# Optimization experiments

Measured on AMD Instinct MI355X. Metric: run time of the kernel, lower is better.

## Reference

```python
import jax, jax.numpy as jnp
import numpy as np

H = 8          # num_heads
WIN = 256      # window_size (even); half-window = 128
NEG = -1e30    # stand-in for -inf that keeps softmax grad finite


def setup_inputs() -> dict:
    key = jax.random.key(0)
    ks = jax.random.split(key, 6)
    B, S, D, E = 2, 2048, 512, 512
    x = jax.random.normal(ks[0], (B, S, D), dtype=jnp.float32)
    padding_mask = jax.random.randint(ks[1], (B, S), 0, 2, dtype=jnp.int32)
    Wqkv = jax.random.normal(ks[2], (3 * E, D), dtype=jnp.float32) * 0.02
    bqkv = jnp.zeros((3 * E,), dtype=jnp.float32)
    Wo = jax.random.normal(ks[3], (E, E), dtype=jnp.float32) * 0.02
    bo = jnp.zeros((E,), dtype=jnp.float32)
    return {"x": x, "padding_mask": padding_mask, "Wqkv": Wqkv, "bqkv": bqkv,
            "Wo": Wo, "bo": bo}


def reference(x, padding_mask, Wqkv, bqkv, Wo, bo):
    B, S, _ = x.shape
    E = Wo.shape[0]
    Dh = E // H
    # qkv projection -> [B, H, S, 3*Dh]
    qkv = (x @ Wqkv.T + bqkv).reshape(B, S, H, 3 * Dh).transpose(0, 2, 1, 3)
    q, k, v = jnp.split(qkv, 3, axis=-1)
    # full S x S scores (original materializes [B,H,S,S]); scale by sqrt(head_dim)
    scores = jnp.einsum('bhsd,bhtd->bhst', q, k) / jnp.sqrt(jnp.float32(Dh))
    # sliding-window band: |i - j| <= window_size // 2
    i = jnp.arange(S)[:, None]
    j = jnp.arange(S)[None, :]
    band = jnp.abs(i - j) <= (WIN // 2)               # [S, S]
    # padding: entry valid only if both row and col tokens are non-pad
    pad = padding_mask.astype(bool)                    # [B, S]
    valid = band[None, None] & pad[:, None, None, :] & pad[:, None, :, None]
    scores = jnp.where(valid, scores, NEG)
    A = jax.nn.softmax(scores, axis=-1)
    # rows with no valid entry -> nan_to_num(., 0) in original -> zeros here
    row_valid = jnp.any(valid, axis=-1, keepdims=True)
    A = jnp.where(row_valid, A, 0.0)
    Y = jnp.einsum('bhst,bhtd->bhsd', A, v)            # [B,H,S,Dh]
    Y = Y.transpose(0, 2, 1, 3).reshape(B, S, E)
    return Y @ Wo.T + bo
```

## Files before the change

kernel.cpp:

```cpp
#include <hip/hip_runtime.h>

#define NH   8
#define SEQ  2048
#define DIM  512
#define EMB  512
#define DH   64
#define HALF 128
#define QT   16
#define KW   272
#define SCS  276

typedef __attribute__((ext_vector_type(8))) short short8;
typedef __attribute__((ext_vector_type(4))) float f32x4;

__device__ __forceinline__ unsigned short f2bf(float f) {
    unsigned int u = __float_as_uint(f);
    return (unsigned short)((u + 0x7fffu + ((u >> 16) & 1u)) >> 16);
}

__device__ __forceinline__ unsigned cvtpk(float lo, float hi) {
    unsigned r;
    asm("v_cvt_pk_bf16_f32 %0, %1, %2" : "=v"(r) : "v"(lo), "v"(hi));
    return r;
}

__device__ __forceinline__ void gload_lds16(const void* g, void* l) {
    __builtin_amdgcn_global_load_lds((__attribute__((address_space(1))) void*)g,
                                     (__attribute__((address_space(3))) void*)l,
                                     16, 0, 0);
}

__global__ __launch_bounds__(256)
void gemm_qkv(const float* __restrict__ A, const float* __restrict__ B,
              const float* __restrict__ bias, unsigned short* __restrict__ qkvh,
              unsigned short* __restrict__ vT) {
    constexpr int BM = 128, BN = 64, BK = 64;
    __shared__ unsigned short As[BM * BK];
    __shared__ unsigned short Bs[BN * BK];
    const int bid = blockIdx.x;
    const int wg = (bid & 7) * 96 + (bid >> 3);
    const int bm = (wg / 24) * BM, bn = (wg % 24) * BN;
    const int t = threadIdx.x, lane = t & 63, wid = t >> 6;
    const int wr = wid >> 1, wc = wid & 1;
    const int lr = lane & 15, lg = lane >> 4;

    f32x4 acc[4][2];
    #pragma unroll
    for (int m = 0; m < 4; ++m)
        #pragma unroll
        for (int n = 0; n < 2; ++n)
            acc[m][n] = (f32x4){0.f, 0.f, 0.f, 0.f};

    for (int kt = 0; kt < DIM; kt += BK) {
        #pragma unroll
        for (int i = 0; i < 4; ++i) {
            const int c = t + 256 * i, r = c >> 3, c8 = c & 7;
            const float4* src = (const float4*)(A + (size_t)(bm + r) * DIM + kt + c8 * 8);
            const float4 v0 = src[0], v1 = src[1];
            const uint4 pk = make_uint4(cvtpk(v0.x, v0.y), cvtpk(v0.z, v0.w),
                                        cvtpk(v1.x, v1.y), cvtpk(v1.z, v1.w));
            *(uint4*)&As[r * 64 + ((c8 ^ (r & 7)) << 3)] = pk;
        }
        #pragma unroll
        for (int i = 0; i < 2; ++i) {
            const int c = t + 256 * i, r = c >> 3, c8 = c & 7;
            const float4* src = (const float4*)(B + (size_t)(bn + r) * DIM + kt + c8 * 8);
            const float4 v0 = src[0], v1 = src[1];
            const uint4 pk = make_uint4(cvtpk(v0.x, v0.y), cvtpk(v0.z, v0.w),
                                        cvtpk(v1.x, v1.y), cvtpk(v1.z, v1.w));
            *(uint4*)&Bs[r * 64 + ((c8 ^ (r & 7)) << 3)] = pk;
        }
        __syncthreads();
        short8 af[2][4], bf[2][2];
        #pragma unroll
        for (int kk = 0; kk < 2; ++kk) {
            #pragma unroll
            for (int m = 0; m < 4; ++m) {
                const int row = wr * 64 + m * 16 + lr;
                af[kk][m] = *(const short8*)&As[row * 64 + (((kk * 4 + lg) ^ (row & 7)) << 3)];
            }
            #pragma unroll
            for (int n = 0; n < 2; ++n) {
                const int row = wc * 32 + n * 16 + lr;
                bf[kk][n] = *(const short8*)&Bs[row * 64 + (((kk * 4 + lg) ^ (row & 7)) << 3)];
            }
        }
        #pragma unroll
        for (int kk = 0; kk < 2; ++kk)
            #pragma unroll
            for (int m = 0; m < 4; ++m)
                #pragma unroll
                for (int n = 0; n < 2; ++n)
                    acc[m][n] = __builtin_amdgcn_mfma_f32_16x16x32_bf16(af[kk][m], bf[kk][n], acc[m][n], 0, 0, 0);
        __syncthreads();
    }

    unsigned short* Tr = As;
    #pragma unroll
    for (int n = 0; n < 2; ++n) {
        const int cl = wc * 32 + n * 16 + lr;
        const float bv = bias[bn + cl];
        #pragma unroll
        for (int m = 0; m < 4; ++m)
            #pragma unroll
            for (int r = 0; r < 4; ++r)
                Tr[(wr * 64 + m * 16 + lg * 4 + r) * 72 + cl] = f2bf(acc[m][n][r] + bv);
    }
    __syncthreads();

    const int h = bn / 192, ty = (bn >> 6) % 3;
    const int bb = bm >> 11, s0 = bm & 2047;
    if (ty < 2) {
        unsigned short* plane = qkvh + (((size_t)(bb * NH + h) * 3 + ty) * SEQ) * DH;
        const int s = t >> 1, hf = (t & 1) * 32;
        unsigned short* dst = plane + (size_t)(s0 + s) * DH + hf;
        #pragma unroll
        for (int k8 = 0; k8 < 4; ++k8)
            *(short8*)&dst[k8 * 8] = *(const short8*)&Tr[s * 72 + hf + k8 * 8];
    } else {
        const int d = t >> 2, pp = t & 3;
        unsigned short* vrow = vT + ((size_t)(bb * NH + h) * DH + d) * SEQ + s0 + pp * 32;
        #pragma unroll
        for (int k8 = 0; k8 < 4; ++k8) {
            alignas(16) unsigned short tmp[8];
            #pragma unroll
            for (int k = 0; k < 8; ++k) tmp[k] = Tr[(pp * 32 + k8 * 8 + k) * 72 + d];
            *(short8*)&vrow[k8 * 8] = *(short8*)tmp;
        }
    }
}

__global__ __launch_bounds__(256)
void attn_mfma(const unsigned short* __restrict__ qkvh,
               const unsigned short* __restrict__ vT,
               const int* __restrict__ pad,
               unsigned short* __restrict__ Yb) {
    const int bid = blockIdx.x;
    const int wg = (bid & 7) * 256 + (bid >> 3);
    const int bh = wg >> 7, qt = wg & 127;
    const int b = bh >> 3, h = bh & 7;
    const int i0 = qt * QT, kb = i0 - HALF;
    const int t = threadIdx.x, lane = t & 63, w = t >> 6;
    const int lr = lane & 15, lg = lane >> 4;

    __shared__ float Sc[QT * SCS];

    const unsigned short* Qg = qkvh + ((size_t)bh * 3 + 0) * SEQ * DH;
    const unsigned short* Kg = qkvh + ((size_t)bh * 3 + 1) * SEQ * DH;
    const unsigned short* vTg = vT + (size_t)bh * DH * SEQ;
    const int* padb = pad + b * SEQ;

    short8 qf[2];
    #pragma unroll
    for (int kk = 0; kk < 2; ++kk)
        qf[kk] = *(const short8*)&Qg[(size_t)(i0 + lr) * DH + kk * 32 + lg * 8];

    const int k0 = w * 16;
    #pragma unroll
    for (int c = 0; c < 5; ++c) {
        const int nc = (c < 4) ? 64 : 16;
        if (k0 < nc) {
            const int jl = c * 64 + k0 + lr;
            const int j = kb + jl;
            const int jc = j < 0 ? 0 : (j > SEQ - 1 ? SEQ - 1 : j);
            const int kv = (j >= 0 && j < SEQ) ? padb[j] : 0;
            f32x4 a0 = (f32x4){0.f, 0.f, 0.f, 0.f};
            #pragma unroll
            for (int kk = 0; kk < 2; ++kk) {
                const short8 bfr = *(const short8*)&Kg[(size_t)jc * DH + kk * 32 + lg * 8];
                a0 = __builtin_amdgcn_mfma_f32_16x16x32_bf16(qf[kk], bfr, a0, 0, 0, 0);
            }
            #pragma unroll
            for (int r = 0; r < 4; ++r) {
                const int q0 = lg * 4 + r;
                const bool ok = kv && (jl >= q0) && (jl <= q0 + 2 * HALF);
                Sc[q0 * SCS + jl] = ok ? a0[r] * 0.125f : -1e30f;
            }
        }
    }
    __syncthreads();

    for (int r = w; r < QT; r += 4) {
        float* row = &Sc[r * SCS];
        unsigned short* prow = (unsigned short*)row;
        if (!padb[i0 + r]) {
            #pragma unroll
            for (int u = 0; u < 5; ++u) {
                const int jl = lane + 64 * u;
                if (jl < KW) prow[jl] = 0;
            }
            if (lane >= 16 && lane < 32) prow[256 + lane] = 0;
            continue;
        }
        float v[5];
        float mx = -1e30f;
        #pragma unroll
        for (int u = 0; u < 5; ++u) {
            const int jl = lane + 64 * u;
            v[u] = (jl < KW) ? row[jl] : -1e30f;
            mx = fmaxf(mx, v[u]);
        }
        #pragma unroll
        for (int off = 32; off; off >>= 1) mx = fmaxf(mx, __shfl_xor(mx, off));
        float s = 0.f;
        #pragma unroll
        for (int u = 0; u < 5; ++u) { v[u] = __expf(v[u] - mx); s += v[u]; }
        #pragma unroll
        for (int off = 32; off; off >>= 1) s += __shfl_xor(s, off);
        const float inv = 1.f / s;
        asm volatile("" ::: "memory");
        #pragma unroll
        for (int u = 0; u < 5; ++u) {
            const int jl = lane + 64 * u;
            if (jl < KW) prow[jl] = f2bf(v[u] * inv);
        }
        if (lane >= 16 && lane < 32) prow[256 + lane] = 0;
    }
    __syncthreads();

    f32x4 o0 = (f32x4){0.f, 0.f, 0.f, 0.f};
    const unsigned short* PbU = (const unsigned short*)Sc;
    const int d0 = w * 16 + lr;
    #pragma unroll
    for (int c = 0; c < 5; ++c) {
        const int nkk = (c < 4) ? 2 : 1;
        #pragma unroll
        for (int kk = 0; kk < nkk; ++kk) {
            int j0 = kb + c * 64 + kk * 32 + lg * 8;
            j0 = j0 < 0 ? 0 : (j0 > SEQ - 8 ? SEQ - 8 : j0);
            const short8 vf = *(const short8*)&vTg[(size_t)d0 * SEQ + j0];
            const short8 pf = *(const short8*)&PbU[lr * (SCS * 2) + c * 64 + kk * 32 + lg * 8];
            o0 = __builtin_amdgcn_mfma_f32_16x16x32_bf16(pf, vf, o0, 0, 0, 0);
        }
    }

    #pragma unroll
    for (int r = 0; r < 4; ++r)
        Yb[(size_t)(b * SEQ + i0 + lg * 4 + r) * EMB + h * DH + d0] = f2bf(o0[r]);
}

__global__ __launch_bounds__(256)
void gemm_out(const unsigned short* __restrict__ A, const float* __restrict__ B,
              const float* __restrict__ bias, float* __restrict__ C) {
    constexpr int BM = 64, BN = 64, BK = 64;
    __shared__ unsigned short As[BM * BK];
    __shared__ unsigned short Bs[BN * BK];
    const int bid = blockIdx.x;
    const int wg = (bid & 7) * 64 + (bid >> 3);
    const int bm = (wg >> 3) * BM, bn = (wg & 7) * BN;
    const int t = threadIdx.x, lane = t & 63, wid = t >> 6;
    const int wr = wid >> 1, wc = wid & 1;
    const int lr = lane & 15, lg = lane >> 4;

    f32x4 acc[2][2];
    #pragma unroll
    for (int m = 0; m < 2; ++m)
        #pragma unroll
        for (int n = 0; n < 2; ++n)
            acc[m][n] = (f32x4){0.f, 0.f, 0.f, 0.f};

    for (int kt = 0; kt < DIM; kt += BK) {
        #pragma unroll
        for (int off = 0; off < BM * BK; off += 2048) {
            const int e = off + t * 8, r = e >> 6, c4 = (e & 63) >> 3;
            const int gc = (c4 ^ (r & 7)) << 3;
            gload_lds16(A + (size_t)(bm + r) * EMB + kt + gc, &As[e]);
        }
        #pragma unroll
        for (int i = 0; i < 2; ++i) {
            const int c = t + 256 * i, r = c >> 3, c8 = c & 7;
            const float4* src = (const float4*)(B + (size_t)(bn + r) * DIM + kt + c8 * 8);
            const float4 v0 = src[0], v1 = src[1];
            const uint4 pk = make_uint4(cvtpk(v0.x, v0.y), cvtpk(v0.z, v0.w),
                                        cvtpk(v1.x, v1.y), cvtpk(v1.z, v1.w));
            *(uint4*)&Bs[r * 64 + ((c8 ^ (r & 7)) << 3)] = pk;
        }
        __syncthreads();
        short8 af[2][2], bf[2][2];
        #pragma unroll
        for (int kk = 0; kk < 2; ++kk) {
            #pragma unroll
            for (int m = 0; m < 2; ++m) {
                const int row = wr * 32 + m * 16 + lr;
                af[kk][m] = *(const short8*)&As[row * BK + (((kk * 4 + lg) ^ (row & 7)) << 3)];
            }
            #pragma unroll
            for (int n = 0; n < 2; ++n) {
                const int row = wc * 32 + n * 16 + lr;
                bf[kk][n] = *(const short8*)&Bs[row * BK + (((kk * 4 + lg) ^ (row & 7)) << 3)];
            }
        }
        #pragma unroll
        for (int kk = 0; kk < 2; ++kk)
            #pragma unroll
            for (int m = 0; m < 2; ++m)
                #pragma unroll
                for (int n = 0; n < 2; ++n)
                    acc[m][n] = __builtin_amdgcn_mfma_f32_16x16x32_bf16(af[kk][m], bf[kk][n], acc[m][n], 0, 0, 0);
        __syncthreads();
    }

    const int orow = bm + wr * 32 + lg * 4;
    const int oc0 = bn + wc * 32 + lr;
    #pragma unroll
    for (int m = 0; m < 2; ++m)
        #pragma unroll
        for (int n = 0; n < 2; ++n) {
            const int col = oc0 + n * 16;
            const float bv = bias[col];
            #pragma unroll
            for (int r = 0; r < 4; ++r)
                C[(size_t)(orow + m * 16 + r) * EMB + col] = acc[m][n][r] + bv;
        }
}

extern "C" void kernel_launch(void* const* d_in, const int* in_sizes, int n_in,
                              void* d_out, int out_size, void* d_ws, size_t ws_size,
                              hipStream_t stream) {
    const float* x    = (const float*)d_in[0];
    const int*   pad  = (const int*)d_in[1];
    const float* Wqkv = (const float*)d_in[2];
    const float* bqkv = (const float*)d_in[3];
    const float* Wo   = (const float*)d_in[4];
    const float* bo   = (const float*)d_in[5];
    float* out = (float*)d_out;

    char* p = (char*)d_ws;
    unsigned short* qkvh = (unsigned short*)p;
    unsigned short* vT   = (unsigned short*)(p + 12582912);
    unsigned short* Yb   = (unsigned short*)(p + 16777216);

    dim3 blk(256);
    gemm_qkv<<<dim3(768), blk, 0, stream>>>(x, Wqkv, bqkv, qkvh, vT);
    attn_mfma<<<dim3(2048), blk, 0, stream>>>(qkvh, vT, pad, Yb);
    gemm_out<<<dim3(512), blk, 0, stream>>>(Yb, Wo, bo, out);
}
```

Before: 56.72 us.

## Double-buffer LDS tiles and prefetch next K-slice in both GEMM kernels

Both projection GEMMs now keep two LDS buffers and load the next K tile's global data into registers, or straight into LDS via global_load_lds, while MFMAs run on the current tile. One barrier per iteration replaces two. The aim is to hide global-load latency behind compute. The cost is double the LDS footprint and extra prefetch registers, which may reduce occupancy. In gemm_out, the async direct-to-LDS A loads rely on the single barrier to be complete before they are read.

```diff
diff --git a/kernel.cpp b/kernel.cpp
--- a/kernel.cpp
+++ b/kernel.cpp
@@ -35,8 +35,8 @@
               const float* __restrict__ bias, unsigned short* __restrict__ qkvh,
               unsigned short* __restrict__ vT) {
     constexpr int BM = 128, BN = 64, BK = 64;
-    __shared__ unsigned short As[BM * BK];
-    __shared__ unsigned short Bs[BN * BK];
+    __shared__ unsigned short As[2][BM * BK];
+    __shared__ unsigned short Bs[2][BN * BK];
     const int bid = blockIdx.x;
     const int wg = (bid & 7) * 96 + (bid >> 3);
     const int bm = (wg / 24) * BM, bn = (wg % 24) * BN;
@@ -51,38 +51,56 @@
         for (int n = 0; n < 2; ++n)
             acc[m][n] = (f32x4){0.f, 0.f, 0.f, 0.f};
 
-    for (int kt = 0; kt < DIM; kt += BK) {
+    float4 rA[4][2], rB[2][2];
+    auto loadA = [&](int kt) {
         #pragma unroll
         for (int i = 0; i < 4; ++i) {
             const int c = t + 256 * i, r = c >> 3, c8 = c & 7;
-            const float4* src = (const float4*)(A + (size_t)(bm + r) * DIM + kt + c8 * 8);
-            const float4 v0 = src[0], v1 = src[1];
-            const uint4 pk = make_uint4(cvtpk(v0.x, v0.y), cvtpk(v0.z, v0.w),
-                                        cvtpk(v1.x, v1.y), cvtpk(v1.z, v1.w));
-            *(uint4*)&As[r * 64 + ((c8 ^ (r & 7)) << 3)] = pk;
-        }
+            const float4* s = (const float4*)(A + (size_t)(bm + r) * DIM + kt + c8 * 8);
+            rA[i][0] = s[0]; rA[i][1] = s[1];
+        }
+    };
+    auto loadB = [&](int kt) {
         #pragma unroll
         for (int i = 0; i < 2; ++i) {
             const int c = t + 256 * i, r = c >> 3, c8 = c & 7;
-            const float4* src = (const float4*)(B + (size_t)(bn + r) * DIM + kt + c8 * 8);
-            const float4 v0 = src[0], v1 = src[1];
-            const uint4 pk = make_uint4(cvtpk(v0.x, v0.y), cvtpk(v0.z, v0.w),
-                                        cvtpk(v1.x, v1.y), cvtpk(v1.z, v1.w));
-            *(uint4*)&Bs[r * 64 + ((c8 ^ (r & 7)) << 3)] = pk;
+            const float4* s = (const float4*)(B + (size_t)(bn + r) * DIM + kt + c8 * 8);
+            rB[i][0] = s[0]; rB[i][1] = s[1];
+        }
+    };
+
+    loadA(0); loadB(0);
+    for (int it = 0; it < 8; ++it) {
+        const int cur = it & 1;
+        #pragma unroll
+        for (int i = 0; i < 4; ++i) {
+            const int c = t + 256 * i, r = c >> 3, c8 = c & 7;
+            const uint4 pk = make_uint4(cvtpk(rA[i][0].x, rA[i][0].y), cvtpk(rA[i][0].z, rA[i][0].w),
+                                        cvtpk(rA[i][1].x, rA[i][1].y), cvtpk(rA[i][1].z, rA[i][1].w));
+            *(uint4*)&As[cur][r * 64 + ((c8 ^ (r & 7)) << 3)] = pk;
+        }
+        #pragma unroll
+        for (int i = 0; i < 2; ++i) {
+            const int c = t + 256 * i, r = c >> 3, c8 = c & 7;
+            const uint4 pk = make_uint4(cvtpk(rB[i][0].x, rB[i][0].y), cvtpk(rB[i][0].z, rB[i][0].w),
+                                        cvtpk(rB[i][1].x, rB[i][1].y), cvtpk(rB[i][1].z, rB[i][1].w));
+            *(uint4*)&Bs[cur][r * 64 + ((c8 ^ (r & 7)) << 3)] = pk;
         }
         __syncthreads();
+        if (it < 7) { loadA((it + 1) * BK); loadB((it + 1) * BK); }
+
         short8 af[2][4], bf[2][2];
         #pragma unroll
         for (int kk = 0; kk < 2; ++kk) {
             #pragma unroll
             for (int m = 0; m < 4; ++m) {
                 const int row = wr * 64 + m * 16 + lr;
-                af[kk][m] = *(const short8*)&As[row * 64 + (((kk * 4 + lg) ^ (row & 7)) << 3)];
+                af[kk][m] = *(const short8*)&As[cur][row * 64 + (((kk * 4 + lg) ^ (row & 7)) << 3)];
             }
             #pragma unroll
             for (int n = 0; n < 2; ++n) {
                 const int row = wc * 32 + n * 16 + lr;
-                bf[kk][n] = *(const short8*)&Bs[row * 64 + (((kk * 4 + lg) ^ (row & 7)) << 3)];
+                bf[kk][n] = *(const short8*)&Bs[cur][row * 64 + (((kk * 4 + lg) ^ (row & 7)) << 3)];
             }
         }
         #pragma unroll
@@ -92,10 +110,10 @@
                 #pragma unroll
                 for (int n = 0; n < 2; ++n)
                     acc[m][n] = __builtin_amdgcn_mfma_f32_16x16x32_bf16(af[kk][m], bf[kk][n], acc[m][n], 0, 0, 0);
-        __syncthreads();
-    }
-
-    unsigned short* Tr = As;
+    }
+    __syncthreads();
+
+    unsigned short* Tr = &As[0][0];
     #pragma unroll
     for (int n = 0; n < 2; ++n) {
         const int cl = wc * 32 + n * 16 + lr;
@@ -243,8 +261,8 @@
 void gemm_out(const unsigned short* __restrict__ A, const float* __restrict__ B,
               const float* __restrict__ bias, float* __restrict__ C) {
     constexpr int BM = 64, BN = 64, BK = 64;
-    __shared__ unsigned short As[BM * BK];
-    __shared__ unsigned short Bs[BN * BK];
+    __shared__ unsigned short As[2][BM * BK];
+    __shared__ unsigned short Bs[2][BN * BK];
     const int bid = blockIdx.x;
     const int wg = (bid & 7) * 64 + (bid >> 3);
     const int bm = (wg >> 3) * BM, bn = (wg & 7) * BN;
@@ -259,35 +277,50 @@
         for (int n = 0; n < 2; ++n)
             acc[m][n] = (f32x4){0.f, 0.f, 0.f, 0.f};
 
-    for (int kt = 0; kt < DIM; kt += BK) {
+    float4 rB[2][2];
+    auto gloadA = [&](int kt, int buf) {
         #pragma unroll
         for (int off = 0; off < BM * BK; off += 2048) {
             const int e = off + t * 8, r = e >> 6, c4 = (e & 63) >> 3;
             const int gc = (c4 ^ (r & 7)) << 3;
-            gload_lds16(A + (size_t)(bm + r) * EMB + kt + gc, &As[e]);
-        }
+            gload_lds16(A + (size_t)(bm + r) * EMB + kt + gc, &As[buf][e]);
+        }
+    };
+    auto loadB = [&](int kt) {
         #pragma unroll
         for (int i = 0; i < 2; ++i) {
             const int c = t + 256 * i, r = c >> 3, c8 = c & 7;
-            const float4* src = (const float4*)(B + (size_t)(bn + r) * DIM + kt + c8 * 8);
-            const float4 v0 = src[0], v1 = src[1];
-            const uint4 pk = make_uint4(cvtpk(v0.x, v0.y), cvtpk(v0.z, v0.w),
-                                        cvtpk(v1.x, v1.y), cvtpk(v1.z, v1.w));
-            *(uint4*)&Bs[r * 64 + ((c8 ^ (r & 7)) << 3)] = pk;
+            const float4* s = (const float4*)(B + (size_t)(bn + r) * DIM + kt + c8 * 8);
+            rB[i][0] = s[0]; rB[i][1] = s[1];
+        }
+    };
+
+    gloadA(0, 0);
+    loadB(0);
+    for (int it = 0; it < 8; ++it) {
+        const int cur = it & 1;
+        #pragma unroll
+        for (int i = 0; i < 2; ++i) {
+            const int c = t + 256 * i, r = c >> 3, c8 = c & 7;
+            const uint4 pk = make_uint4(cvtpk(rB[i][0].x, rB[i][0].y), cvtpk(rB[i][0].z, rB[i][0].w),
+                                        cvtpk(rB[i][1].x, rB[i][1].y), cvtpk(rB[i][1].z, rB[i][1].w));
+            *(uint4*)&Bs[cur][r * 64 + ((c8 ^ (r & 7)) << 3)] = pk;
         }
         __syncthreads();
+        if (it < 7) { gloadA((it + 1) * BK, cur ^ 1); loadB((it + 1) * BK); }
+
         short8 af[2][2], bf[2][2];
         #pragma unroll
         for (int kk = 0; kk < 2; ++kk) {
             #pragma unroll
             for (int m = 0; m < 2; ++m) {
                 const int row = wr * 32 + m * 16 + lr;
-                af[kk][m] = *(const short8*)&As[row * BK + (((kk * 4 + lg) ^ (row & 7)) << 3)];
+                af[kk][m] = *(const short8*)&As[cur][row * BK + (((kk * 4 + lg) ^ (row & 7)) << 3)];
             }
             #pragma unroll
             for (int n = 0; n < 2; ++n) {
                 const int row = wc * 32 + n * 16 + lr;
-                bf[kk][n] = *(const short8*)&Bs[row * BK + (((kk * 4 + lg) ^ (row & 7)) << 3)];
+                bf[kk][n] = *(const short8*)&Bs[cur][row * BK + (((kk * 4 + lg) ^ (row & 7)) << 3)];
             }
         }
         #pragma unroll
@@ -297,7 +330,6 @@
                 #pragma unroll
                 for (int n = 0; n < 2; ++n)
                     acc[m][n] = __builtin_amdgcn_mfma_f32_16x16x32_bf16(af[kk][m], bf[kk][n], acc[m][n], 0, 0, 0);
-        __syncthreads();
     }
 
     const int orow = bm + wr * 32 + lg * 4;
```

After: 56.99 us. Within noise of the previous version (+0.5%).
